# Performance work log

Hardware: AMD Instinct MI355X
Metric: run time of the kernel (lower is better)

## Reference

```python
import jax, jax.numpy as jnp
import numpy as np

NUM_HEADS = 16
WINDOW = 256
DIM = 1024


def setup_inputs() -> dict:
    key = jax.random.key(0)
    k1, k2, k3, k4, k5 = jax.random.split(key, 5)
    B, L, D = 2, 2048, DIM
    s = 1.0 / np.sqrt(D)
    return {
        "x": jax.random.normal(k1, (B, L, D), dtype=jnp.float32),
        "in_proj_w": jax.random.uniform(k2, (3 * D, D), dtype=jnp.float32, minval=-s, maxval=s),
        "in_proj_b": jax.random.uniform(k3, (3 * D,), dtype=jnp.float32, minval=-s, maxval=s),
        "out_w": jax.random.uniform(k4, (D, D), dtype=jnp.float32, minval=-s, maxval=s),
        "out_b": jax.random.uniform(k5, (D,), dtype=jnp.float32, minval=-s, maxval=s),
    }


def reference(x, in_proj_w, in_proj_b, out_w, out_b):
    B, L, D = x.shape
    H = NUM_HEADS
    hd = D // H

    # combined qkv projection, as in nn.MultiheadAttention
    qkv = x @ in_proj_w.T + in_proj_b          # [B, L, 3D]
    q, k, v = jnp.split(qkv, 3, axis=-1)
    q = q.reshape(B, L, H, hd).transpose(0, 2, 1, 3)  # [B, H, L, hd]
    k = k.reshape(B, L, H, hd).transpose(0, 2, 1, 3)
    v = v.reshape(B, L, H, hd).transpose(0, 2, 1, 3)

    scale = 1.0 / jnp.sqrt(jnp.asarray(hd, dtype=x.dtype))
    scores = jnp.einsum("bhqd,bhkd->bhqk", q * scale, k)  # [B, H, L, L]

    # sliding-window causal mask: allowed iff i-window < j <= i
    i = jnp.arange(L)[:, None]
    j = jnp.arange(L)[None, :]
    allowed = (j <= i) & (j > i - WINDOW)                  # [L, L]
    scores = jnp.where(allowed[None, None], scores, -jnp.inf)

    attn = jax.nn.softmax(scores, axis=-1)
    out = jnp.einsum("bhqk,bhkd->bhqd", attn, v)           # [B, H, L, hd]
    out = out.transpose(0, 2, 1, 3).reshape(B, L, D)
    return out @ out_w.T + out_b
```

## Files before the change

kernel.cpp:

```cpp
#include <hip/hip_runtime.h>


#define SEQ_L 2048
#define WIN   256

typedef __bf16 bf16x8 __attribute__((ext_vector_type(8)));
typedef float  f32x4  __attribute__((ext_vector_type(4)));

__device__ __forceinline__ unsigned short f32_to_bf16(float f) {
  unsigned int u = __float_as_uint(f);
  u += 0x7FFFu + ((u >> 16) & 1u);
  return (unsigned short)(u >> 16);
}

__device__ __forceinline__ void async16(const unsigned short* g, unsigned short* l) {
  __builtin_amdgcn_global_load_lds(
      (const __attribute__((address_space(1))) unsigned int*)g,
      (__attribute__((address_space(3))) unsigned int*)l, 16, 0, 0);
}

__global__ void cast_all(const float* __restrict__ x,  unsigned short* __restrict__ xo,
                         const float* __restrict__ w1, unsigned short* __restrict__ w1o,
                         const float* __restrict__ w2, unsigned short* __restrict__ w2o) {
  int i = blockIdx.x * 256 + threadIdx.x;
  const float* in; unsigned short* out; int k;
  if (i < 1048576)       { in = x;  out = xo;  k = i; }
  else if (i < 1835008)  { in = w1; out = w1o; k = i - 1048576; }
  else                   { in = w2; out = w2o; k = i - 1835008; }
  float4 v = ((const float4*)in)[k];
  ushort4 o;
  o.x = f32_to_bf16(v.x); o.y = f32_to_bf16(v.y);
  o.z = f32_to_bf16(v.z); o.w = f32_to_bf16(v.w);
  ((ushort4*)out)[k] = o;
}

template<int TBM, int TBN, int MI, int NI, int OUTBF>
__global__ __launch_bounds__(256) void gemm_nt(
    const unsigned short* __restrict__ A,
    const unsigned short* __restrict__ Bt,
    const float* __restrict__ bias,
    void* __restrict__ Cout, int M, int N, int K)
{
  __shared__ unsigned short As[TBM * 64];
  __shared__ unsigned short Bs[TBN * 64];

  const int tid  = threadIdx.x;
  const int lane = tid & 63;
  const int wave = tid >> 6;
  const int wr   = (wave >> 1) * (MI * 16);
  const int wc   = (wave & 1) * (NI * 16);
  const int quad = lane >> 4;
  const int l16  = lane & 15;
  const int lrow = lane >> 3;
  const int scol = (lane & 7) ^ lrow;

  const long m0 = (long)blockIdx.y * TBM;
  const long n0 = (long)blockIdx.x * TBN;

  f32x4 acc[MI][NI];
#pragma unroll
  for (int i = 0; i < MI; ++i)
#pragma unroll
    for (int j = 0; j < NI; ++j)
#pragma unroll
      for (int r = 0; r < 4; ++r) acc[i][j][r] = 0.0f;

  for (int k0 = 0; k0 < K; k0 += 64) {
#pragma unroll
    for (int p = 0; p < TBM / 32; ++p) {
      int rb = wave * (TBM / 4) + p * 8;
      async16(A + (m0 + rb + lrow) * (long)K + k0 + scol * 8, &As[rb * 64]);
    }
#pragma unroll
    for (int p = 0; p < TBN / 32; ++p) {
      int rb = wave * (TBN / 4) + p * 8;
      async16(Bt + (n0 + rb + lrow) * (long)K + k0 + scol * 8, &Bs[rb * 64]);
    }
    __syncthreads();
#pragma unroll
    for (int ks = 0; ks < 2; ++ks) {
      bf16x8 af[MI], bfv[NI];
#pragma unroll
      for (int mi = 0; mi < MI; ++mi) {
        int r = wr + mi * 16 + l16;
        af[mi] = *(const bf16x8*)(&As[r * 64 + ((ks * 4 + quad) ^ (r & 7)) * 8]);
      }
#pragma unroll
      for (int ni = 0; ni < NI; ++ni) {
        int r = wc + ni * 16 + l16;
        bfv[ni] = *(const bf16x8*)(&Bs[r * 64 + ((ks * 4 + quad) ^ (r & 7)) * 8]);
      }
#pragma unroll
      for (int mi = 0; mi < MI; ++mi)
#pragma unroll
        for (int ni = 0; ni < NI; ++ni)
          acc[mi][ni] = __builtin_amdgcn_mfma_f32_16x16x32_bf16(af[mi], bfv[ni], acc[mi][ni], 0, 0, 0);
    }
    __syncthreads();
  }

#pragma unroll
  for (int ni = 0; ni < NI; ++ni) {
    long col = n0 + wc + ni * 16 + l16;
    float bv = bias[col];
#pragma unroll
    for (int mi = 0; mi < MI; ++mi) {
      long rowb = m0 + wr + mi * 16 + quad * 4;
#pragma unroll
      for (int r = 0; r < 4; ++r) {
        float v = acc[mi][ni][r] + bv;
        if (OUTBF) ((unsigned short*)Cout)[(rowb + r) * N + col] = f32_to_bf16(v);
        else       ((float*)Cout)[(rowb + r) * N + col] = v;
      }
    }
  }
}

__global__ __launch_bounds__(256) void attn_kernel(
    const unsigned short* __restrict__ qkv,
    unsigned short* __restrict__ aout)
{
  __shared__ unsigned short Ks[64 * 72];
  __shared__ unsigned short Vt[64 * 72];
  __shared__ unsigned short Ps[4 * 16 * 72];

  const int tid  = threadIdx.x;
  const int w    = tid >> 6;
  const int lane = tid & 63;
  const int quad = lane >> 4;
  const int l16  = lane & 15;

  const int blk = blockIdx.x;
  const int qb  = blk & 15;
  const int h   = (blk >> 4) & 15;
  const int b   = blk >> 8;

  const int  i0 = qb * 128;
  const long rowbase = (long)b * SEQ_L;

  bf16x8 aq[2][2];
#pragma unroll
  for (int sub = 0; sub < 2; ++sub) {
    const unsigned short* qp =
        qkv + (rowbase + i0 + sub * 64 + w * 16 + l16) * 3072 + h * 64 + quad * 8;
    aq[sub][0] = *(const bf16x8*)(qp);
    aq[sub][1] = *(const bf16x8*)(qp + 32);
  }

  f32x4 o[2][4];
  float l_i[2][4];
#pragma unroll
  for (int sub = 0; sub < 2; ++sub)
#pragma unroll
    for (int ni = 0; ni < 4; ++ni)
#pragma unroll
      for (int r = 0; r < 4; ++r) { o[sub][ni][r] = 0.0f; l_i[sub][r] = 0.0f; }

  unsigned short* psw = &Ps[w * 16 * 72];

  const int j_begin = (i0 >= WIN) ? i0 - WIN : 0;

  for (int j0 = j_begin; j0 < i0 + 128; j0 += 64) {
    __syncthreads();
#pragma unroll
    for (int p = 0; p < 2; ++p) {
      int c = p * 256 + tid, row = c >> 3, col8 = c & 7;
      const unsigned short* base = qkv + (rowbase + j0 + row) * 3072 + h * 64 + col8 * 8;
      *(uint4*)(&Ks[row * 72 + col8 * 8]) = *(const uint4*)(base + 1024);
      unsigned short tmp[8];
      *(uint4*)tmp = *(const uint4*)(base + 2048);
      int rsw = row ^ (col8 << 3);
#pragma unroll
      for (int e = 0; e < 8; ++e)
        Vt[(col8 * 8 + e) * 72 + rsw] = tmp[e];
    }
    __syncthreads();

    bf16x8 kf[4][2];
#pragma unroll
    for (int g = 0; g < 4; ++g) {
      kf[g][0] = *(const bf16x8*)(&Ks[(g * 16 + l16) * 72 + quad * 8]);
      kf[g][1] = *(const bf16x8*)(&Ks[(g * 16 + l16) * 72 + 32 + quad * 8]);
    }
    bf16x8 vf[2][4];
#pragma unroll
    for (int kk = 0; kk < 2; ++kk)
#pragma unroll
      for (int ni = 0; ni < 4; ++ni) {
        int d  = ni * 16 + l16;
        int rb = (kk * 32 + quad * 8) ^ (((d >> 3) & 7) << 3);
        vf[kk][ni] = *(const bf16x8*)(&Vt[d * 72 + rb]);
      }

#pragma unroll
    for (int sub = 0; sub < 2; ++sub) {
      const int i0s = i0 + sub * 64 + w * 16;
      if (j0 > i0s + 15) continue;
      if (j0 + 63 + WIN <= i0s) continue;

      f32x4 s[4];
#pragma unroll
      for (int g = 0; g < 4; ++g) {
        f32x4 z;
#pragma unroll
        for (int r = 0; r < 4; ++r) z[r] = 0.0f;
        z = __builtin_amdgcn_mfma_f32_16x16x32_bf16(aq[sub][0], kf[g][0], z, 0, 0, 0);
        z = __builtin_amdgcn_mfma_f32_16x16x32_bf16(aq[sub][1], kf[g][1], z, 0, 0, 0);
        s[g] = z;
      }
#pragma unroll
      for (int g = 0; g < 4; ++g) {
        int j = j0 + g * 16 + l16;
#pragma unroll
        for (int r = 0; r < 4; ++r) {
          int i = i0s + quad * 4 + r;
          bool ok = (j <= i) && (j > i - WIN);
          float e = ok ? __expf(s[g][r] * 0.125f) : 0.0f;
          psw[(quad * 4 + r) * 72 + g * 16 + l16] = f32_to_bf16(e);
          l_i[sub][r] += e;
        }
      }
      asm volatile("s_waitcnt lgkmcnt(0)" ::: "memory");
#pragma unroll
      for (int kk = 0; kk < 2; ++kk) {
        bf16x8 ap = *(const bf16x8*)(&psw[l16 * 72 + kk * 32 + quad * 8]);
#pragma unroll
        for (int ni = 0; ni < 4; ++ni)
          o[sub][ni] = __builtin_amdgcn_mfma_f32_16x16x32_bf16(ap, vf[kk][ni], o[sub][ni], 0, 0, 0);
      }
    }
  }

#pragma unroll
  for (int sub = 0; sub < 2; ++sub)
#pragma unroll
    for (int r = 0; r < 4; ++r) {
      float rs = l_i[sub][r];
      rs += __shfl_xor(rs, 1);
      rs += __shfl_xor(rs, 2);
      rs += __shfl_xor(rs, 4);
      rs += __shfl_xor(rs, 8);
      float inv_l = 1.0f / rs;
      long row = rowbase + i0 + sub * 64 + w * 16 + quad * 4 + r;
#pragma unroll
      for (int ni = 0; ni < 4; ++ni)
        aout[row * 1024 + h * 64 + ni * 16 + l16] = f32_to_bf16(o[sub][ni][r] * inv_l);
    }
}

extern "C" void kernel_launch(void* const* d_in, const int* in_sizes, int n_in,
                              void* d_out, int out_size, void* d_ws, size_t ws_size,
                              hipStream_t stream)
{
  const float* x  = (const float*)d_in[0];
  const float* w1 = (const float*)d_in[1];
  const float* b1 = (const float*)d_in[2];
  const float* w2 = (const float*)d_in[3];
  const float* b2 = (const float*)d_in[4];
  float* out = (float*)d_out;

  char* ws = (char*)d_ws;
  unsigned short* x_bf   = (unsigned short*)(ws);
  unsigned short* w1_bf  = (unsigned short*)(ws + 8388608);
  unsigned short* w2_bf  = (unsigned short*)(ws + 14680064);
  unsigned short* qkv_bf = (unsigned short*)(ws + 16777216);
  unsigned short* at_bf  = (unsigned short*)(ws + 41943040);

  cast_all<<<8192, 256, 0, stream>>>(x, x_bf, w1, w1_bf, w2, w2_bf);

  dim3 g1(3072 / 128, 4096 / 128);
  gemm_nt<128, 128, 4, 4, 1><<<g1, 256, 0, stream>>>(x_bf, w1_bf, b1, qkv_bf, 4096, 3072, 1024);

  attn_kernel<<<512, 256, 0, stream>>>(qkv_bf, at_bf);

  dim3 g2(1024 / 64, 4096 / 64);
  gemm_nt<64, 64, 2, 2, 0><<<g2, 256, 0, stream>>>(at_bf, w2_bf, b2, out, 4096, 1024, 1024);
}
```

Baseline: 161.9 us.

## Add 256x256 double-buffered 8-wave GEMM for the QKV projection

Replaces the 128x128 single-buffered QKV projection GEMM with a new 256x256-tile kernel using 512 threads, double-buffered LDS, XOR-swizzled layout, and four interleaved compute phases that issue async global-to-LDS loads for upcoming K slices. It uses explicit waitcnt, barriers and setprio to overlap memory traffic with MFMA work. The larger tile raises data reuse. The cost is a grid of only 192 blocks, which underfills 256 CUs, plus 128KB of LDS per block and heavy register pressure.

```diff
diff --git a/kernel.cpp b/kernel.cpp
--- a/kernel.cpp
+++ b/kernel.cpp
@@ -6,6 +6,8 @@
 
 typedef __bf16 bf16x8 __attribute__((ext_vector_type(8)));
 typedef float  f32x4  __attribute__((ext_vector_type(4)));
+
+template<int N> struct ic { static constexpr int v = N; };
 
 __device__ __forceinline__ unsigned short f32_to_bf16(float f) {
   unsigned int u = __float_as_uint(f);
@@ -34,6 +36,142 @@
   ((ushort4*)out)[k] = o;
 }
 
+template<int OUTBF>
+__global__ __launch_bounds__(512, 2) void gemm_nt_256(
+    const unsigned short* __restrict__ A,
+    const unsigned short* __restrict__ Bt,
+    const float* __restrict__ bias,
+    void* __restrict__ Cout, int M, int N, int K)
+{
+  __shared__ unsigned short As[2][256 * 64];
+  __shared__ unsigned short Bs[2][256 * 64];
+
+  const int tid  = threadIdx.x;
+  const int lane = tid & 63;
+  const int w    = tid >> 6;
+  const int wr   = w >> 2;
+  const int wc   = w & 3;
+  const int quad = lane >> 4;
+  const int l16  = lane & 15;
+  const int lrow = lane >> 3 & 7;
+  const int scol = (lane & 7) ^ lrow;
+
+  const long m0 = (long)blockIdx.y * 256;
+  const long n0 = (long)blockIdx.x * 256;
+
+  f32x4 acc[8][4];
+#pragma unroll
+  for (int i = 0; i < 8; ++i)
+#pragma unroll
+    for (int j = 0; j < 4; ++j)
+#pragma unroll
+      for (int r = 0; r < 4; ++r) acc[i][j][r] = 0.0f;
+
+  auto stageA = [&](int buf, int row0, int kc) {
+    async16(A + (m0 + row0 + w * 8 + lrow) * (long)K + kc + scol * 8,
+            &As[buf][(row0 + w * 8) * 64]);
+  };
+  auto stageB = [&](int buf, int b0, int kc) {
+    int wrow = b0 + (w & 3) * 8 + (w >> 2) * 64;
+    async16(Bt + (n0 + wrow + lrow) * (long)K + kc + scol * 8,
+            &Bs[buf][wrow * 64]);
+  };
+  auto hA0 = [&](int buf, int kc) { stageA(buf, 0,  kc); stageA(buf, 128, kc); };
+  auto hA1 = [&](int buf, int kc) { stageA(buf, 64, kc); stageA(buf, 192, kc); };
+  auto hB0 = [&](int buf, int kc) { stageB(buf, 0,  kc); stageB(buf, 128, kc); };
+  auto hB1 = [&](int buf, int kc) { stageB(buf, 32, kc); stageB(buf, 160, kc); };
+
+  auto vmw = [](auto n) {
+    constexpr int V = decltype(n)::v;
+    if constexpr (V == 8)      asm volatile("s_waitcnt vmcnt(8)" ::: "memory");
+    else if constexpr (V == 4) asm volatile("s_waitcnt vmcnt(4)" ::: "memory");
+    else if constexpr (V == 0) asm volatile("s_waitcnt vmcnt(0)" ::: "memory");
+  };
+
+  auto phase = [&](int buf, auto qmc, auto qnc, auto stager, auto v) {
+    constexpr int QM = decltype(qmc)::v, QN = decltype(qnc)::v;
+    bf16x8 af[4][2], bq[2][2];
+    const int rbase = wr * 128 + QM * 64;
+#pragma unroll
+    for (int mi = 0; mi < 4; ++mi) {
+      const int rr = rbase + mi * 16 + l16;
+#pragma unroll
+      for (int kh = 0; kh < 2; ++kh)
+        af[mi][kh] = *(const bf16x8*)&As[buf][rr * 64 + (((kh * 4 + quad) ^ (rr & 7)) << 3)];
+    }
+    const int cbase = wc * 64 + QN * 32;
+#pragma unroll
+    for (int ni = 0; ni < 2; ++ni) {
+      const int rb = cbase + ni * 16 + l16;
+#pragma unroll
+      for (int kh = 0; kh < 2; ++kh)
+        bq[ni][kh] = *(const bf16x8*)&Bs[buf][rb * 64 + (((kh * 4 + quad) ^ (rb & 7)) << 3)];
+    }
+    stager();
+    asm volatile("s_waitcnt lgkmcnt(8)" ::: "memory");
+    __builtin_amdgcn_s_barrier();
+    asm volatile("s_waitcnt lgkmcnt(0)" ::: "memory");
+    __builtin_amdgcn_sched_barrier(0);
+    __builtin_amdgcn_s_setprio(1);
+#pragma unroll
+    for (int kh = 0; kh < 2; ++kh)
+#pragma unroll
+      for (int mi = 0; mi < 4; ++mi)
+#pragma unroll
+        for (int ni = 0; ni < 2; ++ni)
+          acc[QM * 4 + mi][QN * 2 + ni] = __builtin_amdgcn_mfma_f32_16x16x32_bf16(
+              af[mi][kh], bq[ni][kh], acc[QM * 4 + mi][QN * 2 + ni], 0, 0, 0);
+    __builtin_amdgcn_s_setprio(0);
+    vmw(v);
+    __builtin_amdgcn_s_barrier();
+  };
+
+  auto tile = [&](int T, auto s1, auto s34, auto v1, auto v4) {
+    const int buf = T & 1;
+    const int kn1 = (T + 1) << 6;
+    const int kn2 = (T + 2) << 6;
+    phase(buf, ic<0>{}, ic<0>{},
+          [&] { if constexpr (decltype(s1)::v) { hA1(buf ^ 1, kn1); hB1(buf ^ 1, kn1); } }, v1);
+    phase(buf, ic<0>{}, ic<1>{}, [&] {}, ic<-1>{});
+    phase(buf, ic<1>{}, ic<0>{},
+          [&] { if constexpr (decltype(s34)::v) hA0(buf, kn2); }, ic<-1>{});
+    phase(buf, ic<1>{}, ic<1>{},
+          [&] { if constexpr (decltype(s34)::v) hB0(buf, kn2); }, v4);
+  };
+
+  hA0(0, 0); hB0(0, 0); hA1(0, 0); hB1(0, 0); hA0(1, 64); hB0(1, 64);
+  asm volatile("s_waitcnt vmcnt(8)" ::: "memory");
+  __builtin_amdgcn_s_barrier();
+
+  const int NT = K >> 6;
+  int T = 0;
+#pragma unroll 1
+  for (; T < NT - 2; ++T)
+    tile(T, ic<1>{}, ic<1>{}, ic<8>{}, ic<8>{});
+  tile(NT - 2, ic<1>{}, ic<0>{}, ic<8>{}, ic<4>{});
+  tile(NT - 1, ic<0>{}, ic<0>{}, ic<0>{}, ic<-1>{});
+
+#pragma unroll
+  for (int qn = 0; qn < 2; ++qn)
+#pragma unroll
+    for (int ni = 0; ni < 2; ++ni) {
+      long col = n0 + wc * 64 + qn * 32 + ni * 16 + l16;
+      float bv = bias[col];
+#pragma unroll
+      for (int qm = 0; qm < 2; ++qm)
+#pragma unroll
+        for (int mi = 0; mi < 4; ++mi) {
+          long rowb = m0 + wr * 128 + qm * 64 + mi * 16 + quad * 4;
+#pragma unroll
+          for (int r = 0; r < 4; ++r) {
+            float v = acc[qm * 4 + mi][qn * 2 + ni][r] + bv;
+            if (OUTBF) ((unsigned short*)Cout)[(rowb + r) * N + col] = f32_to_bf16(v);
+            else       ((float*)Cout)[(rowb + r) * N + col] = v;
+          }
+        }
+    }
+}
+
 template<int TBM, int TBN, int MI, int NI, int OUTBF>
 __global__ __launch_bounds__(256) void gemm_nt(
     const unsigned short* __restrict__ A,
@@ -268,8 +406,8 @@
 
   cast_all<<<8192, 256, 0, stream>>>(x, x_bf, w1, w1_bf, w2, w2_bf);
 
-  dim3 g1(3072 / 128, 4096 / 128);
-  gemm_nt<128, 128, 4, 4, 1><<<g1, 256, 0, stream>>>(x_bf, w1_bf, b1, qkv_bf, 4096, 3072, 1024);
+  dim3 g1(3072 / 256, 4096 / 256);
+  gemm_nt_256<1><<<g1, 512, 0, stream>>>(x_bf, w1_bf, b1, qkv_bf, 4096, 3072, 1024);
 
   attn_kernel<<<512, 256, 0, stream>>>(qkv_bf, at_bf);
 
```

After: 164.1 us. About the same (+1.4%).

## Add dedicated QKV GEMM with 256x192 tiles and double-buffered async LDS pipeline

Applied to the files above, without the earlier changes.

Replaces the generic 128x128 GEMM for the QKV projection with a specialized 512-thread kernel using 256x192 block tiles, double-buffered LDS filled via global_load_lds, XOR-swizzled shared layout, and explicit vmcnt/lgkmcnt waits interleaved with MFMA clusters and setprio. The aim is to overlap global loads with matrix math and raise data reuse per block. The grid shrinks to 16x16 = 256 blocks, which roughly matches the CU count but may leave a partial wave, and the hand-tuned waitcnt sequence is fragile.

```diff
diff --git a/kernel.cpp b/kernel.cpp
--- a/kernel.cpp
+++ b/kernel.cpp
@@ -6,6 +6,8 @@
 
 typedef __bf16 bf16x8 __attribute__((ext_vector_type(8)));
 typedef float  f32x4  __attribute__((ext_vector_type(4)));
+
+template<int X> struct ic { static constexpr int v = X; };
 
 __device__ __forceinline__ unsigned short f32_to_bf16(float f) {
   unsigned int u = __float_as_uint(f);
@@ -34,6 +36,139 @@
   ((ushort4*)out)[k] = o;
 }
 
+__global__ __launch_bounds__(512, 2) void gemm_qkv(
+    const unsigned short* __restrict__ A,
+    const unsigned short* __restrict__ Bt,
+    const float* __restrict__ bias,
+    unsigned short* __restrict__ C, int M, int N, int K)
+{
+  __shared__ unsigned short As[2][256 * 64];
+  __shared__ unsigned short Bs[2][192 * 64];
+
+  const int tid  = threadIdx.x;
+  const int lane = tid & 63;
+  const int w    = tid >> 6;
+  const int wr   = w >> 2;
+  const int wc   = w & 3;
+  const int quad = lane >> 4;
+  const int l16  = lane & 15;
+  const int lrow = (lane >> 3) & 7;
+  const int scol = (lane & 7) ^ lrow;
+
+  const long m0 = (long)blockIdx.y * 256;
+  const long n0 = (long)blockIdx.x * 192;
+
+  f32x4 acc[8][3];
+#pragma unroll
+  for (int i = 0; i < 8; ++i)
+#pragma unroll
+    for (int j = 0; j < 3; ++j)
+#pragma unroll
+      for (int r = 0; r < 4; ++r) acc[i][j][r] = 0.0f;
+
+  auto stA = [&](int buf, int c, int kc) {
+    async16(A + (m0 + c * 64 + w * 8 + lrow) * (long)K + kc + scol * 8,
+            &As[buf][(c * 64 + w * 8) * 64]);
+  };
+  auto stB = [&](int buf, int c, int kc) {
+    async16(Bt + (n0 + c * 64 + w * 8 + lrow) * (long)K + kc + scol * 8,
+            &Bs[buf][(c * 64 + w * 8) * 64]);
+  };
+  auto hA0 = [&](int buf, int kc) { stA(buf, 0, kc); stA(buf, 2, kc); };
+  auto hA1 = [&](int buf, int kc) { stA(buf, 1, kc); stA(buf, 3, kc); };
+  auto hB  = [&](int buf, int kc) { stB(buf, 0, kc); stB(buf, 1, kc); stB(buf, 2, kc); };
+
+  auto rdA = [&](bf16x8 (&af)[4], int buf, int QM, int kh) {
+#pragma unroll
+    for (int mi = 0; mi < 4; ++mi) {
+      int rr = wr * 128 + QM * 64 + mi * 16 + l16;
+      af[mi] = *(const bf16x8*)&As[buf][rr * 64 + (((kh * 4 + quad) ^ (rr & 7)) << 3)];
+    }
+  };
+  auto rdB = [&](bf16x8 (&bq)[3], int buf, int kh) {
+#pragma unroll
+    for (int ni = 0; ni < 3; ++ni) {
+      int rb = wc * 48 + ni * 16 + l16;
+      bq[ni] = *(const bf16x8*)&Bs[buf][rb * 64 + (((kh * 4 + quad) ^ (rb & 7)) << 3)];
+    }
+  };
+  auto cluster = [&](bf16x8 (&af)[4], bf16x8 (&bq)[3], int mb) {
+    __builtin_amdgcn_s_setprio(1);
+#pragma unroll
+    for (int mi = 0; mi < 4; ++mi)
+#pragma unroll
+      for (int ni = 0; ni < 3; ++ni)
+        acc[mb + mi][ni] = __builtin_amdgcn_mfma_f32_16x16x32_bf16(
+            bq[ni], af[mi], acc[mb + mi][ni], 0, 0, 0);
+    __builtin_amdgcn_s_setprio(0);
+  };
+  auto lgkm0 = [] {
+    asm volatile("s_waitcnt lgkmcnt(0)" ::: "memory");
+    __builtin_amdgcn_sched_barrier(0);
+  };
+  auto vmw = [](auto n) {
+    constexpr int V = decltype(n)::v;
+    if constexpr (V == 7)      asm volatile("s_waitcnt vmcnt(7)" ::: "memory");
+    else if constexpr (V == 2) asm volatile("s_waitcnt vmcnt(2)" ::: "memory");
+    else if constexpr (V == 0) asm volatile("s_waitcnt vmcnt(0)" ::: "memory");
+  };
+
+  hA0(0, 0); hB(0, 0); hA1(0, 0); hA0(1, 64); hB(1, 64);
+  asm volatile("s_waitcnt vmcnt(7)" ::: "memory");
+  __builtin_amdgcn_s_barrier();
+
+  auto tile = [&](int T, auto s1, auto s4, auto v1, auto v4) {
+    const int buf = T & 1;
+    bf16x8 af[4], bq0[3], bq1[3];
+    rdA(af, buf, 0, 0);
+    rdB(bq0, buf, 0);
+    if constexpr (decltype(s1)::v) hA1(buf ^ 1, (T + 1) * 64);
+    lgkm0();
+    cluster(af, bq0, 0);
+    vmw(v1);
+    __builtin_amdgcn_s_barrier();
+    rdA(af, buf, 1, 0);
+    lgkm0();
+    cluster(af, bq0, 4);
+    rdA(af, buf, 0, 1);
+    rdB(bq1, buf, 1);
+    lgkm0();
+    cluster(af, bq1, 0);
+    __builtin_amdgcn_s_barrier();
+    rdA(af, buf, 1, 1);
+    if constexpr (decltype(s4)::v) { hA0(buf, (T + 2) * 64); hB(buf, (T + 2) * 64); }
+    lgkm0();
+    cluster(af, bq1, 4);
+    vmw(v4);
+    __builtin_amdgcn_s_barrier();
+  };
+
+  const int NT = K >> 6;
+#pragma unroll 1
+  for (int T = 0; T < NT - 2; ++T) tile(T, ic<1>{}, ic<1>{}, ic<7>{}, ic<7>{});
+  tile(NT - 2, ic<1>{}, ic<0>{}, ic<7>{}, ic<2>{});
+  tile(NT - 1, ic<0>{}, ic<0>{}, ic<0>{}, ic<-1>{});
+
+#pragma unroll
+  for (int ni = 0; ni < 3; ++ni) {
+    const int nb = wc * 48 + ni * 16 + quad * 4;
+    const float4 bv = *(const float4*)&bias[n0 + nb];
+#pragma unroll
+    for (int qm = 0; qm < 2; ++qm)
+#pragma unroll
+      for (int mi = 0; mi < 4; ++mi) {
+        long m = m0 + wr * 128 + qm * 64 + mi * 16 + l16;
+        f32x4 a = acc[qm * 4 + mi][ni];
+        ushort4 o;
+        o.x = f32_to_bf16(a[0] + bv.x);
+        o.y = f32_to_bf16(a[1] + bv.y);
+        o.z = f32_to_bf16(a[2] + bv.z);
+        o.w = f32_to_bf16(a[3] + bv.w);
+        *(ushort4*)&C[m * (long)N + n0 + nb] = o;
+      }
+  }
+}
+
 template<int TBM, int TBN, int MI, int NI, int OUTBF>
 __global__ __launch_bounds__(256) void gemm_nt(
     const unsigned short* __restrict__ A,
@@ -268,8 +403,8 @@
 
   cast_all<<<8192, 256, 0, stream>>>(x, x_bf, w1, w1_bf, w2, w2_bf);
 
-  dim3 g1(3072 / 128, 4096 / 128);
-  gemm_nt<128, 128, 4, 4, 1><<<g1, 256, 0, stream>>>(x_bf, w1_bf, b1, qkv_bf, 4096, 3072, 1024);
+  dim3 g1(3072 / 192, 4096 / 256);
+  gemm_qkv<<<g1, 512, 0, stream>>>(x_bf, w1_bf, b1, qkv_bf, 4096, 3072, 1024);
 
   attn_kernel<<<512, 256, 0, stream>>>(qkv_bf, at_bf);
 
```

Measured after the change: 155.0 us (median of 4 runs). -4.2%, faster.
